# Performance work log

Measured on AMD Instinct MI355X. Metric: run time of the kernel, lower is better.

The kernel has to match this reference:

```python
import jax, jax.numpy as jnp
import numpy as np

B, T, D, H = 2, 2048, 1024, 16
HD = D // H
SCALE = HD ** -0.5


def setup_inputs() -> dict:
    key = jax.random.key(0)
    k1, k2, k3 = jax.random.split(key, 3)
    x = jax.random.normal(k1, (B, T, D), dtype=jnp.float32)
    w_qkv = jax.random.normal(k2, (D, 3 * D), dtype=jnp.float32) * (D ** -0.5)
    w_proj = jax.random.normal(k3, (D, D), dtype=jnp.float32) * (D ** -0.5)
    b_proj = jnp.zeros((D,), dtype=jnp.float32)
    return {"x": x, "w_qkv": w_qkv, "w_proj": w_proj, "b_proj": b_proj}


def reference(x, w_qkv, w_proj, b_proj):
    b, t, d = x.shape
    qkv = jnp.einsum('btd,de->bte', x, w_qkv)            # [B,T,3D]
    qkv = qkv.reshape(b, t, 3, H, HD)
    q = qkv[:, :, 0].transpose(0, 2, 1, 3)               # [B,H,T,HD]
    k = qkv[:, :, 1].transpose(0, 2, 1, 3)
    v = qkv[:, :, 2].transpose(0, 2, 1, 3)
    scores = jnp.einsum('bhqd,bhkd->bhqk', q, k) * SCALE  # [B,H,T,T]
    # NOTE: faithful to the source, softmax over dim=1 (the HEAD axis)
    probs = jax.nn.softmax(scores, axis=1)
    attn_out = jnp.einsum('bhqk,bhkd->bhqd', probs, v)
    attn_out = attn_out.transpose(0, 2, 1, 3).reshape(b, t, d)
    out = jnp.einsum('btd,de->bte', attn_out, w_proj) + b_proj
    return out
```

## Files before the change

kernel.cpp:

```cpp
#include <hip/hip_runtime.h>
#include <hip/hip_bf16.h>
#include <stdint.h>

typedef __bf16 bf16;
typedef __attribute__((ext_vector_type(8))) __bf16 bf16x8;
typedef __attribute__((ext_vector_type(4))) __bf16 bf16x4;
typedef __attribute__((ext_vector_type(4))) float f32x4;

#define MFMA_16x16x32(a, b, c) __builtin_amdgcn_mfma_f32_16x16x32_bf16((a), (b), (c), 0, 0, 0)

__device__ __forceinline__ void gld_lds16(const void* g, void* l) {
    __builtin_amdgcn_global_load_lds(
        (const __attribute__((address_space(1))) void*)g,
        (__attribute__((address_space(3))) void*)l,
        16, 0, 0);
}

__global__ void cvt_f32_bf16(const float* __restrict__ in, bf16* __restrict__ out, int n) {
    int i = (blockIdx.x * blockDim.x + threadIdx.x) * 8;
    if (i >= n) return;
    f32x4 a = *(const f32x4*)(in + i);
    f32x4 b = *(const f32x4*)(in + i + 4);
    bf16x8 o;
#pragma unroll
    for (int j = 0; j < 4; ++j) { o[j] = (bf16)a[j]; o[j + 4] = (bf16)b[j]; }
    *(bf16x8*)(out + i) = o;
}

__global__ void transpose_cvt(const float* __restrict__ in, bf16* __restrict__ out, int R, int C) {
    __shared__ float tile[32][33];
    int c0 = blockIdx.x * 32, r0 = blockIdx.y * 32;
    int tc = threadIdx.x & 31, tr = threadIdx.x >> 5;
#pragma unroll
    for (int i = 0; i < 4; ++i) {
        int r = tr + i * 8;
        tile[r][tc] = in[(size_t)(r0 + r) * C + c0 + tc];
    }
    __syncthreads();
#pragma unroll
    for (int i = 0; i < 4; ++i) {
        int r = tr + i * 8;
        out[(size_t)(c0 + r) * R + r0 + tc] = (bf16)tile[tc][r];
    }
}

template <int EPI>
__global__ void __launch_bounds__(256) gemm_bf16(
    const bf16* __restrict__ A, const bf16* __restrict__ Bt, int M, int N, int K,
    float* __restrict__ Cf, const float* __restrict__ bias,
    bf16* __restrict__ q_out, bf16* __restrict__ k_out, bf16* __restrict__ v_out)
{
    __shared__ bf16 As[128 * 32];
    __shared__ bf16 Bs[128 * 32];
    const int t = threadIdx.x, w = t >> 6, l = t & 63;
    const int l15 = l & 15, lh = l >> 4;
    const int m0 = blockIdx.y * 128, n0 = blockIdx.x * 128;
    const int wm = w >> 1, wn = w & 1;

    const int srow = w * 16 + (l >> 2);
    const int scol = (l & 3) * 8;
    const bf16* gA = A + (size_t)(m0 + srow) * K + scol;
    const bf16* gB = Bt + (size_t)(n0 + srow) * K + scol;
    char* lA = (char*)As + w * 1024;
    char* lB = (char*)Bs + w * 1024;

    f32x4 acc[4][4] = {};

    for (int kt = 0; kt < K; kt += 32) {
        __syncthreads();
        gld_lds16(gA + kt, lA);
        gld_lds16(gA + (size_t)64 * K + kt, lA + 4096);
        gld_lds16(gB + kt, lB);
        gld_lds16(gB + (size_t)64 * K + kt, lB + 4096);
        asm volatile("s_waitcnt vmcnt(0)" ::: "memory");
        __syncthreads();

        const bf16* pa = As + (wm * 64 + l15) * 32 + lh * 8;
        const bf16* pb = Bs + (wn * 64 + l15) * 32 + lh * 8;
        bf16x8 af[4], bfr[4];
#pragma unroll
        for (int i = 0; i < 4; ++i) {
            af[i]  = *(const bf16x8*)(pa + i * 512);
            bfr[i] = *(const bf16x8*)(pb + i * 512);
        }
#pragma unroll
        for (int mi = 0; mi < 4; ++mi)
#pragma unroll
            for (int ni = 0; ni < 4; ++ni)
                acc[mi][ni] = MFMA_16x16x32(af[mi], bfr[ni], acc[mi][ni]);
    }

    if (EPI == 1) {
#pragma unroll
        for (int ni = 0; ni < 4; ++ni) {
            int n = n0 + wn * 64 + ni * 16 + l15;
            float bb = bias[n];
#pragma unroll
            for (int mi = 0; mi < 4; ++mi)
#pragma unroll
                for (int r = 0; r < 4; ++r) {
                    int m = m0 + wm * 64 + mi * 16 + lh * 4 + r;
                    Cf[(size_t)m * N + n] = acc[mi][ni][r] + bb;
                }
        }
    } else {
        const int which = n0 >> 10;
#pragma unroll
        for (int ni = 0; ni < 4; ++ni) {
            int n = n0 + wn * 64 + ni * 16 + l15;
            int h = (n >> 6) & 15;
            int d = n & 63;
#pragma unroll
            for (int mi = 0; mi < 4; ++mi)
#pragma unroll
                for (int r = 0; r < 4; ++r) {
                    int m = m0 + wm * 64 + mi * 16 + lh * 4 + r;
                    int b = m >> 11, tt = m & 2047;
                    bf16 val = (bf16)acc[mi][ni][r];
                    size_t hb = (size_t)b * 16 + h;
                    if (which == 0)      q_out[(hb * 2048 + tt) * 64 + d] = val;
                    else if (which == 1) k_out[(hb * 2048 + tt) * 64 + d] = val;
                    else                 v_out[(hb * 64 + d) * 2048 + tt] = val;
                }
        }
    }
}

__global__ void __launch_bounds__(1024, 4) attn_kernel(
    const bf16* __restrict__ Q, const bf16* __restrict__ Kmat, const bf16* __restrict__ Vt,
    bf16* __restrict__ p0, bf16* __restrict__ p1, bf16* __restrict__ p2, bf16* __restrict__ p3)
{
    __shared__ bf16 S[16][32][136];
    __shared__ bf16 invS[32][136];
    const int t = threadIdx.x;
    const int w = t >> 6;
    const int l = t & 63;
    const int l15 = l & 15, lh = l >> 4;

    const int bid = blockIdx.x;
    const int b = (bid & 7) >> 2;
    const int ks = bid & 3;
    const int qt = (bid >> 3) * 32;

    const size_t headQK = ((size_t)b * 16 + w) * (2048 * 64);
    const size_t headV  = ((size_t)b * 16 + w) * (64 * 2048);
    const float SCL = 0.125f * 1.44269504089f;

    bf16x8 qf[2][2];
#pragma unroll
    for (int qb2 = 0; qb2 < 2; ++qb2)
#pragma unroll
        for (int dc = 0; dc < 2; ++dc)
            qf[qb2][dc] = *(const bf16x8*)(Q + headQK + (size_t)(qt + qb2 * 16 + l15) * 64 + dc * 32 + lh * 8);

    f32x4 o[2][4] = {};

    for (int it = 0; it < 4; ++it) {
        const int kt = ks * 512 + it * 128;
        __syncthreads();
#pragma unroll
        for (int kb = 0; kb < 8; ++kb) {
            const bf16* kp = Kmat + headQK + (size_t)(kt + kb * 16 + l15) * 64 + lh * 8;
            bf16x8 ak0 = *(const bf16x8*)(kp);
            bf16x8 ak1 = *(const bf16x8*)(kp + 32);
#pragma unroll
            for (int qb2 = 0; qb2 < 2; ++qb2) {
                f32x4 s = {};
                s = MFMA_16x16x32(ak0, qf[qb2][0], s);
                s = MFMA_16x16x32(ak1, qf[qb2][1], s);
                bf16x4 pk;
#pragma unroll
                for (int r = 0; r < 4; ++r)
                    pk[r] = (bf16)exp2f(s[r] * SCL);
                *(bf16x4*)&S[w][qb2 * 16 + l15][kb * 16 + lh * 4] = pk;
            }
        }
        __syncthreads();
        {
            const int sq = t >> 5, kq = (t & 31) * 4;
            float a0 = 0.f, a1 = 0.f, a2 = 0.f, a3 = 0.f;
#pragma unroll
            for (int hh = 0; hh < 16; ++hh) {
                bf16x4 e4 = *(const bf16x4*)&S[hh][sq][kq];
                a0 += (float)e4[0]; a1 += (float)e4[1];
                a2 += (float)e4[2]; a3 += (float)e4[3];
            }
            bf16x4 iv;
            iv[0] = (bf16)__builtin_amdgcn_rcpf(a0);
            iv[1] = (bf16)__builtin_amdgcn_rcpf(a1);
            iv[2] = (bf16)__builtin_amdgcn_rcpf(a2);
            iv[3] = (bf16)__builtin_amdgcn_rcpf(a3);
            *(bf16x4*)&invS[sq][kq] = iv;
        }
        __syncthreads();
#pragma unroll
        for (int ksub = 0; ksub < 4; ++ksub) {
            bf16x8 bv[4];
#pragma unroll
            for (int ni = 0; ni < 4; ++ni)
                bv[ni] = *(const bf16x8*)(Vt + headV + (size_t)(ni * 16 + l15) * 2048 + kt + ksub * 32 + lh * 8);
#pragma unroll
            for (int qb2 = 0; qb2 < 2; ++qb2) {
                bf16x8 ev  = *(const bf16x8*)(&S[w][qb2 * 16 + l15][ksub * 32 + lh * 8]);
                bf16x8 ivv = *(const bf16x8*)(&invS[qb2 * 16 + l15][ksub * 32 + lh * 8]);
                bf16x8 ap;
#pragma unroll
                for (int j = 0; j < 8; ++j)
                    ap[j] = (bf16)((float)ev[j] * (float)ivv[j]);
#pragma unroll
                for (int ni = 0; ni < 4; ++ni)
                    o[qb2][ni] = MFMA_16x16x32(ap, bv[ni], o[qb2][ni]);
            }
        }
    }
    bf16* dst = (ks == 0 ? p0 : ks == 1 ? p1 : ks == 2 ? p2 : p3) + (size_t)b * (2048 * 1024);
#pragma unroll
    for (int qb2 = 0; qb2 < 2; ++qb2)
#pragma unroll
        for (int ni = 0; ni < 4; ++ni)
#pragma unroll
            for (int r = 0; r < 4; ++r) {
                int tt = qt + qb2 * 16 + lh * 4 + r;
                int d = ni * 16 + l15;
                dst[(size_t)tt * 1024 + w * 64 + d] = (bf16)o[qb2][ni][r];
            }
}

__global__ void reduce_part4(const bf16* __restrict__ p0, const bf16* __restrict__ p1,
                             const bf16* __restrict__ p2, const bf16* __restrict__ p3,
                             bf16* __restrict__ out, int n) {
    int i = (blockIdx.x * blockDim.x + threadIdx.x) * 8;
    if (i >= n) return;
    bf16x8 a = *(const bf16x8*)(p0 + i);
    bf16x8 b = *(const bf16x8*)(p1 + i);
    bf16x8 c = *(const bf16x8*)(p2 + i);
    bf16x8 d = *(const bf16x8*)(p3 + i);
    bf16x8 o;
#pragma unroll
    for (int j = 0; j < 8; ++j)
        o[j] = (bf16)(((float)a[j] + (float)b[j]) + ((float)c[j] + (float)d[j]));
    *(bf16x8*)(out + i) = o;
}

extern "C" void kernel_launch(void* const* d_in, const int* in_sizes, int n_in,
                              void* d_out, int out_size, void* d_ws, size_t ws_size,
                              hipStream_t stream)
{
    const float* x      = (const float*)d_in[0];
    const float* w_qkv  = (const float*)d_in[1];
    const float* w_proj = (const float*)d_in[2];
    const float* b_proj = (const float*)d_in[3];
    float* out = (float*)d_out;

    char* ws = (char*)d_ws;
    const size_t MB = 1048576;
    bf16* wprojT = (bf16*)(ws + 0 * MB);
    bf16* xb     = (bf16*)(ws + 2 * MB);
    bf16* wqkvT  = (bf16*)(ws + 10 * MB);
    bf16* qb     = (bf16*)(ws + 18 * MB);
    bf16* kb     = (bf16*)(ws + 26 * MB);
    bf16* vt     = (bf16*)(ws + 34 * MB);
    bf16* part0  = (bf16*)(ws + 2 * MB);
    bf16* part1  = (bf16*)(ws + 10 * MB);
    bf16* part2  = (bf16*)(ws + 42 * MB);
    bf16* part3  = (bf16*)(ws + 50 * MB);
    bf16* attnb  = (bf16*)(ws + 2 * MB);

    cvt_f32_bf16<<<2048, 256, 0, stream>>>(x, xb, 4194304);
    transpose_cvt<<<dim3(96, 32), 256, 0, stream>>>(w_qkv, wqkvT, 1024, 3072);
    transpose_cvt<<<dim3(32, 32), 256, 0, stream>>>(w_proj, wprojT, 1024, 1024);

    gemm_bf16<0><<<dim3(24, 32), 256, 0, stream>>>(xb, wqkvT, 4096, 3072, 1024,
                                                   nullptr, nullptr, qb, kb, vt);
    attn_kernel<<<512, 1024, 0, stream>>>(qb, kb, vt, part0, part1, part2, part3);
    reduce_part4<<<2048, 256, 0, stream>>>(part0, part1, part2, part3, attnb, 4194304);
    gemm_bf16<1><<<dim3(8, 32), 256, 0, stream>>>(attnb, wprojT, 4096, 1024, 1024,
                                                  out, b_proj, nullptr, nullptr, nullptr);

    (void)in_sizes; (void)n_in; (void)out_size; (void)ws_size;
}
```

Before: 228.3 us.

## Double-buffer attention score tiles and normalize probabilities in place

The attention kernel now works on 64-key chunks in a double-buffered LDS score array, so PV for one chunk overlaps with score computation for the next. Fewer barriers are needed per chunk. The head-axis softmax normalization is written back into the score buffer in place, which removes the separate invS array and the per-element multiply in the PV loop. The softmax scale (times log2e) is folded into Q at the QKV GEMM epilogue, so the kernel uses the raw exp2 intrinsic. The cost is more loop iterations with smaller tiles, plus an extra LDS write pass in the normalization step.

```diff
diff --git a/kernel.cpp b/kernel.cpp
--- a/kernel.cpp
+++ b/kernel.cpp
@@ -5,6 +5,7 @@
 typedef __bf16 bf16;
 typedef __attribute__((ext_vector_type(8))) __bf16 bf16x8;
 typedef __attribute__((ext_vector_type(4))) __bf16 bf16x4;
+typedef __attribute__((ext_vector_type(2))) __bf16 bf16x2;
 typedef __attribute__((ext_vector_type(4))) float f32x4;
 
 #define MFMA_16x16x32(a, b, c) __builtin_amdgcn_mfma_f32_16x16x32_bf16((a), (b), (c), 0, 0, 0)
@@ -105,6 +106,7 @@
         }
     } else {
         const int which = n0 >> 10;
+        const float QSCL = 0.125f * 1.44269504089f;
 #pragma unroll
         for (int ni = 0; ni < 4; ++ni) {
             int n = n0 + wn * 64 + ni * 16 + l15;
@@ -116,11 +118,11 @@
                 for (int r = 0; r < 4; ++r) {
                     int m = m0 + wm * 64 + mi * 16 + lh * 4 + r;
                     int b = m >> 11, tt = m & 2047;
-                    bf16 val = (bf16)acc[mi][ni][r];
+                    float av = acc[mi][ni][r];
                     size_t hb = (size_t)b * 16 + h;
-                    if (which == 0)      q_out[(hb * 2048 + tt) * 64 + d] = val;
-                    else if (which == 1) k_out[(hb * 2048 + tt) * 64 + d] = val;
-                    else                 v_out[(hb * 64 + d) * 2048 + tt] = val;
+                    if (which == 0)      q_out[(hb * 2048 + tt) * 64 + d] = (bf16)(av * QSCL);
+                    else if (which == 1) k_out[(hb * 2048 + tt) * 64 + d] = (bf16)av;
+                    else                 v_out[(hb * 64 + d) * 2048 + tt] = (bf16)av;
                 }
         }
     }
@@ -130,8 +132,7 @@
     const bf16* __restrict__ Q, const bf16* __restrict__ Kmat, const bf16* __restrict__ Vt,
     bf16* __restrict__ p0, bf16* __restrict__ p1, bf16* __restrict__ p2, bf16* __restrict__ p3)
 {
-    __shared__ bf16 S[16][32][136];
-    __shared__ bf16 invS[32][136];
+    __shared__ bf16 S[2][16][32][72];
     const int t = threadIdx.x;
     const int w = t >> 6;
     const int l = t & 63;
@@ -144,7 +145,6 @@
 
     const size_t headQK = ((size_t)b * 16 + w) * (2048 * 64);
     const size_t headV  = ((size_t)b * 16 + w) * (64 * 2048);
-    const float SCL = 0.125f * 1.44269504089f;
 
     bf16x8 qf[2][2];
 #pragma unroll
@@ -155,11 +155,10 @@
 
     f32x4 o[2][4] = {};
 
-    for (int it = 0; it < 4; ++it) {
-        const int kt = ks * 512 + it * 128;
-        __syncthreads();
-#pragma unroll
-        for (int kb = 0; kb < 8; ++kb) {
+    auto SCORE = [&](int g, int buf) {
+        const int kt = ks * 512 + g * 64;
+#pragma unroll
+        for (int kb = 0; kb < 4; ++kb) {
             const bf16* kp = Kmat + headQK + (size_t)(kt + kb * 16 + l15) * 64 + lh * 8;
             bf16x8 ak0 = *(const bf16x8*)(kp);
             bf16x8 ak1 = *(const bf16x8*)(kp + 32);
@@ -171,48 +170,62 @@
                 bf16x4 pk;
 #pragma unroll
                 for (int r = 0; r < 4; ++r)
-                    pk[r] = (bf16)exp2f(s[r] * SCL);
-                *(bf16x4*)&S[w][qb2 * 16 + l15][kb * 16 + lh * 4] = pk;
+                    pk[r] = (bf16)__builtin_amdgcn_exp2f(s[r]);
+                *(bf16x4*)&S[buf][w][qb2 * 16 + l15][kb * 16 + lh * 4] = pk;
             }
         }
-        __syncthreads();
-        {
-            const int sq = t >> 5, kq = (t & 31) * 4;
-            float a0 = 0.f, a1 = 0.f, a2 = 0.f, a3 = 0.f;
-#pragma unroll
-            for (int hh = 0; hh < 16; ++hh) {
-                bf16x4 e4 = *(const bf16x4*)&S[hh][sq][kq];
-                a0 += (float)e4[0]; a1 += (float)e4[1];
-                a2 += (float)e4[2]; a3 += (float)e4[3];
-            }
-            bf16x4 iv;
-            iv[0] = (bf16)__builtin_amdgcn_rcpf(a0);
-            iv[1] = (bf16)__builtin_amdgcn_rcpf(a1);
-            iv[2] = (bf16)__builtin_amdgcn_rcpf(a2);
-            iv[3] = (bf16)__builtin_amdgcn_rcpf(a3);
-            *(bf16x4*)&invS[sq][kq] = iv;
-        }
-        __syncthreads();
-#pragma unroll
-        for (int ksub = 0; ksub < 4; ++ksub) {
+    };
+    auto SUMNORM = [&](int buf) {
+        const int sq = t >> 5, kc = (t & 31) * 2;
+        float e0[16], e1[16];
+        float s0 = 0.f, s1 = 0.f;
+#pragma unroll
+        for (int hh = 0; hh < 16; ++hh) {
+            bf16x2 pr = *(const bf16x2*)&S[buf][hh][sq][kc];
+            e0[hh] = (float)pr[0]; e1[hh] = (float)pr[1];
+            s0 += e0[hh]; s1 += e1[hh];
+        }
+        float iv0 = __builtin_amdgcn_rcpf(s0);
+        float iv1 = __builtin_amdgcn_rcpf(s1);
+#pragma unroll
+        for (int hh = 0; hh < 16; ++hh) {
+            bf16x2 pv;
+            pv[0] = (bf16)(e0[hh] * iv0);
+            pv[1] = (bf16)(e1[hh] * iv1);
+            *(bf16x2*)&S[buf][hh][sq][kc] = pv;
+        }
+    };
+    auto PV = [&](int g, int buf) {
+        const int kt = ks * 512 + g * 64;
+#pragma unroll
+        for (int ksub = 0; ksub < 2; ++ksub) {
             bf16x8 bv[4];
 #pragma unroll
             for (int ni = 0; ni < 4; ++ni)
                 bv[ni] = *(const bf16x8*)(Vt + headV + (size_t)(ni * 16 + l15) * 2048 + kt + ksub * 32 + lh * 8);
 #pragma unroll
             for (int qb2 = 0; qb2 < 2; ++qb2) {
-                bf16x8 ev  = *(const bf16x8*)(&S[w][qb2 * 16 + l15][ksub * 32 + lh * 8]);
-                bf16x8 ivv = *(const bf16x8*)(&invS[qb2 * 16 + l15][ksub * 32 + lh * 8]);
-                bf16x8 ap;
-#pragma unroll
-                for (int j = 0; j < 8; ++j)
-                    ap[j] = (bf16)((float)ev[j] * (float)ivv[j]);
+                bf16x8 ap = *(const bf16x8*)(&S[buf][w][qb2 * 16 + l15][ksub * 32 + lh * 8]);
 #pragma unroll
                 for (int ni = 0; ni < 4; ++ni)
                     o[qb2][ni] = MFMA_16x16x32(ap, bv[ni], o[qb2][ni]);
             }
         }
-    }
+    };
+
+    SCORE(0, 0);
+    __syncthreads();
+    SUMNORM(0);
+    __syncthreads();
+    for (int g = 1; g < 8; ++g) {
+        PV(g - 1, (g - 1) & 1);
+        SCORE(g, g & 1);
+        __syncthreads();
+        SUMNORM(g & 1);
+        __syncthreads();
+    }
+    PV(7, 1);
+
     bf16* dst = (ks == 0 ? p0 : ks == 1 ? p1 : ks == 2 ? p2 : p3) + (size_t)b * (2048 * 1024);
 #pragma unroll
     for (int qb2 = 0; qb2 < 2; ++qb2)
```

After: 238.4 us. 1.04x slower.
